# Performance work log

Hardware: AMD Instinct MI355X
Metric: run time of the kernel (lower is better)

The kernel has to match this reference:

```python
import jax, jax.numpy as jnp
import numpy as np
import math

B, T, D_MODEL, N_HEADS = 2, 2048, 2048, 16
D_HEAD = D_MODEL // N_HEADS
ROPE_THETA = 10000.0


def setup_inputs() -> dict:
    key = jax.random.key(0)
    ks = jax.random.split(key, 4)
    x = jax.random.normal(ks[0], (B, T, D_MODEL), dtype=jnp.float32)
    # causal mask: True = masked (matches torch masked_fill semantics)
    mask = jnp.triu(jnp.ones((T, T), dtype=bool), k=1)[None, None]  # [1,1,T,T]
    # rotary freqs: complex freqs_cis = exp(i * t * theta^(-2j/d)) -> cos/sin parts
    inv_freq = 1.0 / (ROPE_THETA ** (jnp.arange(0, D_HEAD, 2, dtype=jnp.float32) / D_HEAD))
    angles = jnp.arange(T, dtype=jnp.float32)[:, None] * inv_freq[None, :]  # [T, D_HEAD//2]
    freqs_cos = jnp.cos(angles)
    freqs_sin = jnp.sin(angles)
    s = 1.0 / math.sqrt(D_MODEL)
    Wqkv = jax.random.normal(ks[1], (D_MODEL, 3 * D_MODEL), dtype=jnp.float32) * s
    bqkv = jnp.zeros((3 * D_MODEL,), dtype=jnp.float32)
    Wproj = jax.random.normal(ks[2], (D_MODEL, D_MODEL), dtype=jnp.float32) * s
    bproj = jnp.zeros((D_MODEL,), dtype=jnp.float32)
    return {"x": x, "mask": mask, "freqs_cos": freqs_cos, "freqs_sin": freqs_sin,
            "Wqkv": Wqkv, "bqkv": bqkv, "Wproj": Wproj, "bproj": bproj}


def _rope(t, cos, sin):
    # t: [B,H,T,D]; cos/sin: [1,1,T,D//2]. Complex multiply on (even, odd) pairs.
    t2 = t.reshape(*t.shape[:-1], -1, 2)
    t_re, t_im = t2[..., 0], t2[..., 1]
    out_re = t_re * cos - t_im * sin
    out_im = t_re * sin + t_im * cos
    return jnp.stack([out_re, out_im], axis=-1).reshape(t.shape)


def reference(x, mask, freqs_cos, freqs_sin, Wqkv, bqkv, Wproj, bproj):
    Bb, Tt, C = x.shape
    qkv = x @ Wqkv + bqkv                                   # [B,T,3C]
    q, k, v = jnp.split(qkv, 3, axis=-1)
    def heads(t):
        return t.reshape(Bb, Tt, N_HEADS, D_HEAD).transpose(0, 2, 1, 3)  # [B,H,T,D]
    q, k, v = heads(q), heads(k), heads(v)
    cos = freqs_cos[None, None]                              # [1,1,T,D//2]
    sin = freqs_sin[None, None]
    q = _rope(q, cos, sin)
    k = _rope(k, cos, sin)
    att = jnp.einsum('bhqd,bhkd->bhqk', q, k) / math.sqrt(D_HEAD)
    att = jnp.where(mask, -jnp.inf, att)
    att = jax.nn.softmax(att, axis=-1)
    # attn_dropout is identity in eval mode
    out = jnp.einsum('bhqk,bhkd->bhqd', att, v)              # [B,H,T,D]
    out = out.transpose(0, 2, 1, 3).reshape(Bb, Tt, C)
    return (out @ Wproj + bproj, k, v)
```

## Files before the change

kernel.cpp:

```cpp
#include <hip/hip_runtime.h>
#include <hip/hip_bf16.h>

#define T_SEQ 2048
#define DM    2048
#define NH    16
#define DH    128
#define NBH   32
#define MROWS 4096

typedef __bf16 bf16x8 __attribute__((ext_vector_type(8)));
typedef __bf16 bf16x4 __attribute__((ext_vector_type(4)));
typedef float  f32x4  __attribute__((ext_vector_type(4)));

#define MFMA16 __builtin_amdgcn_mfma_f32_16x16x32_bf16

__device__ __forceinline__ void async_copy16(const void* g, void* l) {
  __builtin_amdgcn_global_load_lds((const __attribute__((address_space(1))) void*)g,
                                   (__attribute__((address_space(3))) void*)l, 16, 0, 0);
}


__global__ void cast_bf16_k(const float* __restrict__ x, __bf16* __restrict__ xb) {
  int i = (blockIdx.x * 256 + threadIdx.x) * 4;
  float4 v = *reinterpret_cast<const float4*>(x + i);
  bf16x4 o;
  o[0] = (__bf16)v.x; o[1] = (__bf16)v.y; o[2] = (__bf16)v.z; o[3] = (__bf16)v.w;
  *reinterpret_cast<bf16x4*>(xb + i) = o;
}

__global__ void transpose_cast_w(const float* __restrict__ W, __bf16* __restrict__ WT,
                                 int K, int N) {
  __shared__ float tile[32][33];
  int n0 = blockIdx.x * 32, k0 = blockIdx.y * 32;
  int tx = threadIdx.x, ty = threadIdx.y;
  #pragma unroll
  for (int i = 0; i < 4; i++)
    tile[ty + i * 8][tx] = W[(size_t)(k0 + ty + i * 8) * N + n0 + tx];
  __syncthreads();
  #pragma unroll
  for (int i = 0; i < 4; i++)
    WT[(size_t)(n0 + ty + i * 8) * K + k0 + tx] = (__bf16)tile[tx][ty + i * 8];
}

__global__ void transpose_v(const __bf16* __restrict__ Vb, __bf16* __restrict__ Vtb) {
  __shared__ __bf16 tile[32][34];
  int t0 = blockIdx.x * 32, d0 = blockIdx.y * 32, bh = blockIdx.z;
  const __bf16* src = Vb + (size_t)bh * T_SEQ * DH;
  __bf16* dst = Vtb + (size_t)bh * DH * T_SEQ;
  int tx = threadIdx.x, ty = threadIdx.y;
  #pragma unroll
  for (int i = 0; i < 4; i++)
    tile[ty + i * 8][tx] = src[(size_t)(t0 + ty + i * 8) * DH + d0 + tx];
  __syncthreads();
  #pragma unroll
  for (int i = 0; i < 4; i++)
    dst[(size_t)(d0 + ty + i * 8) * T_SEQ + t0 + tx] = tile[tx][ty + i * 8];
}


__device__ __forceinline__ bf16x8 rds(const __bf16* base, int row, int chunk) {
  return *reinterpret_cast<const bf16x8*>(
      reinterpret_cast<const char*>(base) + row * 128 + ((chunk ^ (row & 7)) << 4));
}

__device__ __forceinline__ void stage64(const __bf16* g, int K, int kt, char* lds,
                                        int wave, int lane) {
  #pragma unroll
  for (int j = 0; j < 4; j++) {
    int r = wave * 32 + j * 8 + (lane >> 3);
    int c = lane & 7;
    const char* src = (const char*)g + (size_t)r * (K * 2) + kt * 128 + ((c ^ (r & 7)) << 4);
    async_copy16(src, lds + wave * 4096 + j * 1024);
  }
}

template <int EPI>
__global__ __launch_bounds__(256, 2) void gemm_bt(
    const __bf16* __restrict__ A, const __bf16* __restrict__ Bt, int K,
    const float* __restrict__ bias,
    const float* __restrict__ fcos, const float* __restrict__ fsin,
    __bf16* __restrict__ Qb, __bf16* __restrict__ Kb, __bf16* __restrict__ Vb,
    float* __restrict__ kout, float* __restrict__ vout,
    float* __restrict__ outp) {
  __shared__ __align__(16) char smem[65536];
  const int tid = threadIdx.x, lane = tid & 63, wave = tid >> 6;
  const int hi = lane >> 4, lo = lane & 15;
  const int wm = (wave >> 1) * 64, wn = (wave & 1) * 64;
  const __bf16* Ab = A + (size_t)blockIdx.y * 128 * K;
  const __bf16* Bb = Bt + (size_t)blockIdx.x * 128 * K;
  f32x4 acc[4][4] = {};
  const int NK = K >> 6;

  stage64(Ab, K, 0, smem, wave, lane);
  stage64(Bb, K, 0, smem + 32768, wave, lane);
  __syncthreads();

  for (int t = 0; t < NK; ++t) {
    const int sel = (t & 1) ? 16384 : 0;
    const __bf16* Ac = (const __bf16*)(smem + sel);
    const __bf16* Bc = (const __bf16*)(smem + 32768 + sel);
    if (t + 1 < NK) {
      stage64(Ab, K, t + 1, smem + (sel ^ 16384), wave, lane);
      stage64(Bb, K, t + 1, smem + 32768 + (sel ^ 16384), wave, lane);
    }
    bf16x8 a0[4], b0[4], a1[4], b1[4];
    #pragma unroll
    for (int m = 0; m < 4; ++m) a0[m] = rds(Ac, wm + m * 16 + lo, hi);
    #pragma unroll
    for (int n = 0; n < 4; ++n) b0[n] = rds(Bc, wn + n * 16 + lo, hi);
    __builtin_amdgcn_s_setprio(1);
    #pragma unroll
    for (int m = 0; m < 4; ++m)
      #pragma unroll
      for (int n = 0; n < 4; ++n)
        acc[m][n] = MFMA16(a0[m], b0[n], acc[m][n], 0, 0, 0);
    __builtin_amdgcn_s_setprio(0);
    #pragma unroll
    for (int m = 0; m < 4; ++m) a1[m] = rds(Ac, wm + m * 16 + lo, 4 + hi);
    #pragma unroll
    for (int n = 0; n < 4; ++n) b1[n] = rds(Bc, wn + n * 16 + lo, 4 + hi);
    __builtin_amdgcn_s_setprio(1);
    #pragma unroll
    for (int m = 0; m < 4; ++m)
      #pragma unroll
      for (int n = 0; n < 4; ++n)
        acc[m][n] = MFMA16(a1[m], b1[n], acc[m][n], 0, 0, 0);
    __builtin_amdgcn_s_setprio(0);
    __syncthreads();
  }

  float* sc = (float*)smem;
  const int rl_r = tid >> 3;
  const int cb   = (tid & 7) * 16;
  #pragma unroll
  for (int cc = 0; cc < 4; ++cc) {
    __syncthreads();
    if ((wave >> 1) == (cc >> 1)) {
      #pragma unroll
      for (int mm = 0; mm < 2; ++mm) {
        int m = (cc & 1) * 2 + mm;
        #pragma unroll
        for (int j = 0; j < 4; ++j) {
          int col = wn + j * 16 + lo;
          int rl = mm * 16 + hi * 4;
          #pragma unroll
          for (int r = 0; r < 4; ++r)
            sc[(rl + r) * 132 + col] = acc[m][j][r];
        }
      }
    }
    __syncthreads();
    float v[16];
    #pragma unroll
    for (int q = 0; q < 4; ++q)
      *reinterpret_cast<float4*>(&v[q * 4]) =
          *reinterpret_cast<const float4*>(&sc[rl_r * 132 + cb + q * 4]);
    const int row = blockIdx.y * 128 + cc * 32 + rl_r;
    const int n0  = blockIdx.x * 128 + cb;
    #pragma unroll
    for (int q = 0; q < 4; ++q) {
      float4 bv = *reinterpret_cast<const float4*>(&bias[n0 + q * 4]);
      v[q * 4 + 0] += bv.x; v[q * 4 + 1] += bv.y;
      v[q * 4 + 2] += bv.z; v[q * 4 + 3] += bv.w;
    }
    if (EPI == 1) {
      const int which = n0 >> 11;
      const int wn2 = n0 & 2047, h = wn2 >> 7, d0 = wn2 & 127;
      const int b = row >> 11, tt = row & 2047;
      if (which < 2) {
        const float* cp = fcos + tt * 64 + (d0 >> 1);
        const float* sp = fsin + tt * 64 + (d0 >> 1);
        float4 c0 = *reinterpret_cast<const float4*>(cp);
        float4 c1 = *reinterpret_cast<const float4*>(cp + 4);
        float4 s0 = *reinterpret_cast<const float4*>(sp);
        float4 s1 = *reinterpret_cast<const float4*>(sp + 4);
        float cs[8] = {c0.x, c0.y, c0.z, c0.w, c1.x, c1.y, c1.z, c1.w};
        float sn[8] = {s0.x, s0.y, s0.z, s0.w, s1.x, s1.y, s1.z, s1.w};
        #pragma unroll
        for (int p = 0; p < 8; ++p) {
          float re = v[2 * p], im = v[2 * p + 1];
          v[2 * p]     = re * cs[p] - im * sn[p];
          v[2 * p + 1] = re * sn[p] + im * cs[p];
        }
      }
      size_t base = (((size_t)(b * NH + h)) * T_SEQ + tt) * DH + d0;
      bf16x8 o0, o1;
      #pragma unroll
      for (int p = 0; p < 8; ++p) { o0[p] = (__bf16)v[p]; o1[p] = (__bf16)v[8 + p]; }
      if (which == 0) {
        *reinterpret_cast<bf16x8*>(Qb + base) = o0;
        *reinterpret_cast<bf16x8*>(Qb + base + 8) = o1;
      } else if (which == 1) {
        *reinterpret_cast<bf16x8*>(Kb + base) = o0;
        *reinterpret_cast<bf16x8*>(Kb + base + 8) = o1;
        #pragma unroll
        for (int q = 0; q < 4; ++q)
          *reinterpret_cast<float4*>(kout + base + q * 4) =
              *reinterpret_cast<const float4*>(&v[q * 4]);
      } else {
        *reinterpret_cast<bf16x8*>(Vb + base) = o0;
        *reinterpret_cast<bf16x8*>(Vb + base + 8) = o1;
        #pragma unroll
        for (int q = 0; q < 4; ++q)
          *reinterpret_cast<float4*>(vout + base + q * 4) =
              *reinterpret_cast<const float4*>(&v[q * 4]);
      }
    } else {
      float* op = outp + (size_t)row * DM + n0;
      #pragma unroll
      for (int q = 0; q < 4; ++q)
        *reinterpret_cast<float4*>(op + q * 4) =
            *reinterpret_cast<const float4*>(&v[q * 4]);
    }
  }
}


__device__ __forceinline__ bf16x8 lds_frag(const __bf16* base, int row, int chunk) {
  return *reinterpret_cast<const bf16x8*>(
      reinterpret_cast<const char*>(base) + row * 256 + ((chunk ^ (row & 7)) << 4));
}

__device__ __forceinline__ void stage64x256(const __bf16* g, __bf16* lds, int tid) {
  const int wave = tid >> 6, lane = tid & 63;
  #pragma unroll
  for (int j = 0; j < 4; j++) {
    int off = j * 4096 + wave * 1024;
    int r = (off >> 8) + (lane >> 4);
    int c = lane & 15;
    const char* gs = (const char*)g + (size_t)r * 256 + ((c ^ (r & 7)) << 4);
    async_copy16(gs, (char*)lds + off);
  }
}

__device__ __forceinline__ void stage128x128(const __bf16* g, size_t rstrideB, int colB,
                                             __bf16* lds, int tid) {
  const int wave = tid >> 6, lane = tid & 63;
  #pragma unroll
  for (int j = 0; j < 4; j++) {
    int off = j * 4096 + wave * 1024;
    int r = (off >> 7) + (lane >> 3);
    int c = lane & 7;
    const char* gs = (const char*)g + (size_t)r * rstrideB + colB + ((c ^ (r & 7)) << 4);
    async_copy16(gs, (char*)lds + off);
  }
}

__global__ __launch_bounds__(256, 2) void attn_fwd(
    const __bf16* __restrict__ Qb, const __bf16* __restrict__ Kb,
    const __bf16* __restrict__ Vtb, __bf16* __restrict__ att_out) {
  __shared__ __bf16 Ks[64 * 128];
  __shared__ __bf16 Vts[128 * 64];
  __shared__ __bf16 Ps[4 * 16 * 64];
  const int tid = threadIdx.x, lane = tid & 63, wave = tid >> 6;
  const int hi = lane >> 4, lo = lane & 15;
  const int linear = (int)blockIdx.x;
  const int xcd = linear & 7, rest = linear >> 3;
  const int bh = xcd + 8 * (rest >> 4);
  const int pair = rest & 15;
  const int b = bh >> 4, h = bh & 15;
  const __bf16* Qg = Qb + (size_t)bh * T_SEQ * DH;
  const __bf16* Kg = Kb + (size_t)bh * T_SEQ * DH;
  const __bf16* Vg = Vtb + (size_t)bh * DH * T_SEQ;
  const float scale = 0.08838834764831845f;
  const float L2E = 1.4426950408889634f;
  __bf16* Pw = Ps + wave * 1024;

  for (int pass = 0; pass < 2; ++pass) {
    const int qj = pass ? (31 - pair) : pair;
    const int q0 = qj * 64;
    const int qg = q0 + wave * 16 + lo;
    bf16x8 qf[4];
    const __bf16* qp = Qg + (size_t)qg * DH + hi * 8;
    #pragma unroll
    for (int ks = 0; ks < 4; ++ks) qf[ks] = *reinterpret_cast<const bf16x8*>(qp + ks * 32);
    f32x4 oacc[8] = {};
    float m = -3e38f, l = 0.f;
    const int NT = qj + 1;

    for (int kt = 0; kt < NT; ++kt) {
      __syncthreads();
      stage64x256(Kg + (size_t)kt * 64 * DH, Ks, tid);
      stage128x128(Vg, (size_t)T_SEQ * 2, kt * 128, Vts, tid);
      __syncthreads();

      f32x4 sacc[4] = {};
      __builtin_amdgcn_s_setprio(1);
      #pragma unroll
      for (int ks = 0; ks < 4; ++ks)
        #pragma unroll
        for (int sf = 0; sf < 4; ++sf) {
          bf16x8 ak = lds_frag(Ks, sf * 16 + lo, ks * 4 + hi);
          sacc[sf] = MFMA16(ak, qf[ks], sacc[sf], 0, 0, 0);
        }
      __builtin_amdgcn_s_setprio(0);
      const bool diag = (kt == NT - 1);
      float mx = -3e38f;
      #pragma unroll
      for (int sf = 0; sf < 4; ++sf)
        #pragma unroll
        for (int r = 0; r < 4; ++r) {
          float v = sacc[sf][r] * scale;
          if (diag && (kt * 64 + sf * 16 + hi * 4 + r) > qg) v = -3e38f;
          sacc[sf][r] = v;
          mx = fmaxf(mx, v);
        }
      mx = fmaxf(mx, __shfl_xor(mx, 16, 64));
      mx = fmaxf(mx, __shfl_xor(mx, 32, 64));
      const bool nr = __all(mx - m <= 8.0f);
      if (!nr) {
        float mnew = fmaxf(m, mx);
        float alpha = __builtin_exp2f((m - mnew) * L2E);
        m = mnew;
        l *= alpha;
        #pragma unroll
        for (int df = 0; df < 8; ++df) {
          oacc[df][0] *= alpha; oacc[df][1] *= alpha;
          oacc[df][2] *= alpha; oacc[df][3] *= alpha;
        }
      }
      float rs = 0.f;
      #pragma unroll
      for (int sf = 0; sf < 4; ++sf)
        #pragma unroll
        for (int r = 0; r < 4; ++r) {
          float p = __builtin_exp2f((sacc[sf][r] - m) * L2E);
          sacc[sf][r] = p;
          rs += p;
        }
      rs += __shfl_xor(rs, 16, 64);
      rs += __shfl_xor(rs, 32, 64);
      l += rs;
      #pragma unroll
      for (int sf = 0; sf < 4; ++sf) {
        bf16x4 pk;
        pk[0] = (__bf16)sacc[sf][0]; pk[1] = (__bf16)sacc[sf][1];
        pk[2] = (__bf16)sacc[sf][2]; pk[3] = (__bf16)sacc[sf][3];
        int byte = sf * 32 + hi * 8;
        int chunk = byte >> 4, rem = byte & 15;
        char* p = (char*)Pw + lo * 128 + (((chunk ^ (lo & 7)) << 4) | rem);
        *reinterpret_cast<bf16x4*>(p) = pk;
      }
      __builtin_amdgcn_s_setprio(1);
      #pragma unroll
      for (int ks = 0; ks < 2; ++ks) {
        bf16x8 bp = rds(Pw, lo, ks * 4 + hi);
        #pragma unroll
        for (int df = 0; df < 8; ++df) {
          bf16x8 av = rds(Vts, df * 16 + lo, ks * 4 + hi);
          oacc[df] = MFMA16(av, bp, oacc[df], 0, 0, 0);
        }
      }
      __builtin_amdgcn_s_setprio(0);
    }

    float inv = 1.0f / l;
    int qrow = b * T_SEQ + q0 + wave * 16 + lo;
    #pragma unroll
    for (int df = 0; df < 8; ++df) {
      bf16x4 pk;
      pk[0] = (__bf16)(oacc[df][0] * inv);
      pk[1] = (__bf16)(oacc[df][1] * inv);
      pk[2] = (__bf16)(oacc[df][2] * inv);
      pk[3] = (__bf16)(oacc[df][3] * inv);
      int d = df * 16 + hi * 4;
      *reinterpret_cast<bf16x4*>(att_out + (size_t)qrow * DM + h * DH + d) = pk;
    }
  }
}


extern "C" void kernel_launch(void* const* d_in, const int* in_sizes, int n_in,
                              void* d_out, int out_size, void* d_ws, size_t ws_size,
                              hipStream_t stream) {
  const float* x     = (const float*)d_in[0];
  const float* fcos  = (const float*)d_in[2];
  const float* fsin  = (const float*)d_in[3];
  const float* Wqkv  = (const float*)d_in[4];
  const float* bqkv  = (const float*)d_in[5];
  const float* Wproj = (const float*)d_in[6];
  const float* bproj = (const float*)d_in[7];
  float* out  = (float*)d_out;
  float* kout = out + (size_t)8388608;
  float* vout = out + (size_t)16777216;

  char* ws = (char*)d_ws;
  __bf16* xb     = (__bf16*)(ws);
  __bf16* WqkvT  = (__bf16*)(ws + 16777216);
  __bf16* WprojT = (__bf16*)(ws + 41943040);
  __bf16* Qb     = (__bf16*)(ws + 50331648);
  __bf16* Kb     = (__bf16*)(ws + 67108864);
  __bf16* Vb     = (__bf16*)(ws + 83886080);
  __bf16* Vtb    = (__bf16*)(ws + 100663296);
  __bf16* att    = xb;

  cast_bf16_k<<<8192, 256, 0, stream>>>(x, xb);
  transpose_cast_w<<<dim3(192, 64), dim3(32, 8), 0, stream>>>(Wqkv, WqkvT, DM, 3 * DM);
  transpose_cast_w<<<dim3(64, 64), dim3(32, 8), 0, stream>>>(Wproj, WprojT, DM, DM);
  gemm_bt<1><<<dim3(48, 32), 256, 0, stream>>>(xb, WqkvT, DM, bqkv, fcos, fsin,
                                               Qb, Kb, Vb, kout, vout, nullptr);
  transpose_v<<<dim3(64, 4, NBH), dim3(32, 8), 0, stream>>>(Vb, Vtb);
  attn_fwd<<<512, 256, 0, stream>>>(Qb, Kb, Vtb, att);
  gemm_bt<0><<<dim3(16, 32), 256, 0, stream>>>(att, WprojT, DM, bproj, nullptr, nullptr,
                                               nullptr, nullptr, nullptr, nullptr, nullptr, out);
}
```

Measured before the change: 281.6 us.

## Prefetch next K/V tile into registers to overlap global loads with compute

Replaces the direct global-to-LDS async copies of each K and V tile with register-staged loads. The next tile is fetched from global memory into registers while the current tile is being computed, then written to LDS at the top of the next iteration. This hides global-memory latency behind the QK and PV MFMA work. In exchange it uses 8 more vector registers per thread for staging, which under the (256,2) launch bounds could cause spills, and it adds explicit LDS store instructions.

```diff
diff --git a/kernel.cpp b/kernel.cpp
--- a/kernel.cpp
+++ b/kernel.cpp
@@ -221,29 +221,39 @@
       reinterpret_cast<const char*>(base) + row * 256 + ((chunk ^ (row & 7)) << 4));
 }
 
-__device__ __forceinline__ void stage64x256(const __bf16* g, __bf16* lds, int tid) {
-  const int wave = tid >> 6, lane = tid & 63;
+__device__ __forceinline__ void ldK(const __bf16* Kg, int kt, int wave, int lane,
+                                    bf16x8 k[4]) {
+  const char* g = (const char*)(Kg + (size_t)kt * 64 * DH);
   #pragma unroll
   for (int j = 0; j < 4; j++) {
     int off = j * 4096 + wave * 1024;
     int r = (off >> 8) + (lane >> 4);
     int c = lane & 15;
-    const char* gs = (const char*)g + (size_t)r * 256 + ((c ^ (r & 7)) << 4);
-    async_copy16(gs, (char*)lds + off);
-  }
-}
-
-__device__ __forceinline__ void stage128x128(const __bf16* g, size_t rstrideB, int colB,
-                                             __bf16* lds, int tid) {
-  const int wave = tid >> 6, lane = tid & 63;
+    k[j] = *reinterpret_cast<const bf16x8*>(g + (size_t)r * 256 + ((c ^ (r & 7)) << 4));
+  }
+}
+
+__device__ __forceinline__ void ldV(const __bf16* Vg, int kt, int wave, int lane,
+                                    bf16x8 v[4]) {
+  const char* g = (const char*)Vg;
+  const int colB = kt * 128;
   #pragma unroll
   for (int j = 0; j < 4; j++) {
     int off = j * 4096 + wave * 1024;
     int r = (off >> 7) + (lane >> 3);
     int c = lane & 7;
-    const char* gs = (const char*)g + (size_t)r * rstrideB + colB + ((c ^ (r & 7)) << 4);
-    async_copy16(gs, (char*)lds + off);
-  }
+    v[j] = *reinterpret_cast<const bf16x8*>(g + (size_t)r * (T_SEQ * 2) + colB + ((c ^ (r & 7)) << 4));
+  }
+}
+
+__device__ __forceinline__ void commitKV(__bf16* Ks, __bf16* Vts, int wave, int lane,
+                                         const bf16x8 k[4], const bf16x8 v[4]) {
+  #pragma unroll
+  for (int j = 0; j < 4; j++)
+    *reinterpret_cast<bf16x8*>((char*)Ks + j * 4096 + wave * 1024 + lane * 16) = k[j];
+  #pragma unroll
+  for (int j = 0; j < 4; j++)
+    *reinterpret_cast<bf16x8*>((char*)Vts + j * 4096 + wave * 1024 + lane * 16) = v[j];
 }
 
 __global__ __launch_bounds__(256, 2) void attn_fwd(
@@ -278,11 +288,18 @@
     float m = -3e38f, l = 0.f;
     const int NT = qj + 1;
 
+    bf16x8 kst[4], vst[4];
+    ldK(Kg, 0, wave, lane, kst);
+    ldV(Vg, 0, wave, lane, vst);
+
     for (int kt = 0; kt < NT; ++kt) {
       __syncthreads();
-      stage64x256(Kg + (size_t)kt * 64 * DH, Ks, tid);
-      stage128x128(Vg, (size_t)T_SEQ * 2, kt * 128, Vts, tid);
+      commitKV(Ks, Vts, wave, lane, kst, vst);
       __syncthreads();
+      if (kt + 1 < NT) {
+        ldK(Kg, kt + 1, wave, lane, kst);
+        ldV(Vg, kt + 1, wave, lane, vst);
+      }
 
       f32x4 sacc[4] = {};
       __builtin_amdgcn_s_setprio(1);
```

After: 276.9 us. About the same (-1.7%).

## Give each attention wave two query fragments and split query tiles across blocks

Applied to the files above, without the earlier changes.

The attention kernel now launches 1024 blocks of 2 waves instead of 512 blocks of 4 waves. Each wave handles 32 query rows as two 16-row fragments, so every K and V fragment read from LDS feeds two MFMAs. Each block processes one query tile instead of a balanced pair of tiles, with slot interleaving used to spread causal work. This aims to cut LDS read traffic per MFMA, at the cost of more registers per wave, fewer waves to share each staging step, and possibly worse load balance since blocks now carry uneven causal work.

```diff
diff --git a/kernel.cpp b/kernel.cpp
--- a/kernel.cpp
+++ b/kernel.cpp
@@ -221,11 +221,10 @@
       reinterpret_cast<const char*>(base) + row * 256 + ((chunk ^ (row & 7)) << 4));
 }
 
-__device__ __forceinline__ void stage64x256(const __bf16* g, __bf16* lds, int tid) {
-  const int wave = tid >> 6, lane = tid & 63;
-  #pragma unroll
-  for (int j = 0; j < 4; j++) {
-    int off = j * 4096 + wave * 1024;
+__device__ __forceinline__ void stageK(const __bf16* g, __bf16* lds, int wave, int lane) {
+  #pragma unroll
+  for (int j = 0; j < 8; j++) {
+    int off = j * 2048 + wave * 1024;
     int r = (off >> 8) + (lane >> 4);
     int c = lane & 15;
     const char* gs = (const char*)g + (size_t)r * 256 + ((c ^ (r & 7)) << 4);
@@ -233,136 +232,153 @@
   }
 }
 
-__device__ __forceinline__ void stage128x128(const __bf16* g, size_t rstrideB, int colB,
-                                             __bf16* lds, int tid) {
-  const int wave = tid >> 6, lane = tid & 63;
-  #pragma unroll
-  for (int j = 0; j < 4; j++) {
-    int off = j * 4096 + wave * 1024;
+__device__ __forceinline__ void stageV(const __bf16* g, int kt, __bf16* lds,
+                                       int wave, int lane) {
+  #pragma unroll
+  for (int j = 0; j < 8; j++) {
+    int off = j * 2048 + wave * 1024;
     int r = (off >> 7) + (lane >> 3);
     int c = lane & 7;
-    const char* gs = (const char*)g + (size_t)r * rstrideB + colB + ((c ^ (r & 7)) << 4);
+    const char* gs = (const char*)g + (size_t)r * (T_SEQ * 2) + kt * 128 + ((c ^ (r & 7)) << 4);
     async_copy16(gs, (char*)lds + off);
   }
 }
 
-__global__ __launch_bounds__(256, 2) void attn_fwd(
+__global__ __launch_bounds__(128, 2) void attn_fwd(
     const __bf16* __restrict__ Qb, const __bf16* __restrict__ Kb,
     const __bf16* __restrict__ Vtb, __bf16* __restrict__ att_out) {
   __shared__ __bf16 Ks[64 * 128];
   __shared__ __bf16 Vts[128 * 64];
-  __shared__ __bf16 Ps[4 * 16 * 64];
+  __shared__ __bf16 Ps[2 * 32 * 64];
   const int tid = threadIdx.x, lane = tid & 63, wave = tid >> 6;
   const int hi = lane >> 4, lo = lane & 15;
   const int linear = (int)blockIdx.x;
   const int xcd = linear & 7, rest = linear >> 3;
-  const int bh = xcd + 8 * (rest >> 4);
-  const int pair = rest & 15;
+  const int slot = rest & 31;
+  const int bh = xcd + 8 * (rest >> 5);
+  const int qj = (slot & 1) ? (31 - (slot >> 1)) : (slot >> 1);
   const int b = bh >> 4, h = bh & 15;
   const __bf16* Qg = Qb + (size_t)bh * T_SEQ * DH;
   const __bf16* Kg = Kb + (size_t)bh * T_SEQ * DH;
   const __bf16* Vg = Vtb + (size_t)bh * DH * T_SEQ;
   const float scale = 0.08838834764831845f;
   const float L2E = 1.4426950408889634f;
-  __bf16* Pw = Ps + wave * 1024;
-
-  for (int pass = 0; pass < 2; ++pass) {
-    const int qj = pass ? (31 - pair) : pair;
-    const int q0 = qj * 64;
-    const int qg = q0 + wave * 16 + lo;
-    bf16x8 qf[4];
-    const __bf16* qp = Qg + (size_t)qg * DH + hi * 8;
-    #pragma unroll
-    for (int ks = 0; ks < 4; ++ks) qf[ks] = *reinterpret_cast<const bf16x8*>(qp + ks * 32);
-    f32x4 oacc[8] = {};
-    float m = -3e38f, l = 0.f;
-    const int NT = qj + 1;
-
-    for (int kt = 0; kt < NT; ++kt) {
-      __syncthreads();
-      stage64x256(Kg + (size_t)kt * 64 * DH, Ks, tid);
-      stage128x128(Vg, (size_t)T_SEQ * 2, kt * 128, Vts, tid);
-      __syncthreads();
-
-      f32x4 sacc[4] = {};
-      __builtin_amdgcn_s_setprio(1);
-      #pragma unroll
-      for (int ks = 0; ks < 4; ++ks)
-        #pragma unroll
-        for (int sf = 0; sf < 4; ++sf) {
-          bf16x8 ak = lds_frag(Ks, sf * 16 + lo, ks * 4 + hi);
-          sacc[sf] = MFMA16(ak, qf[ks], sacc[sf], 0, 0, 0);
-        }
-      __builtin_amdgcn_s_setprio(0);
-      const bool diag = (kt == NT - 1);
+  __bf16* Pw = Ps + wave * 2048;
+
+  const int q0 = qj * 64;
+  const int qg0 = q0 + wave * 32 + lo;
+  const int qg1 = qg0 + 16;
+  bf16x8 qf0[4], qf1[4];
+  {
+    const __bf16* qp0 = Qg + (size_t)qg0 * DH + hi * 8;
+    const __bf16* qp1 = Qg + (size_t)qg1 * DH + hi * 8;
+    #pragma unroll
+    for (int ks = 0; ks < 4; ++ks) {
+      qf0[ks] = *reinterpret_cast<const bf16x8*>(qp0 + ks * 32);
+      qf1[ks] = *reinterpret_cast<const bf16x8*>(qp1 + ks * 32);
+    }
+  }
+  f32x4 oacc[8][2] = {};
+  float m0 = -3e38f, m1 = -3e38f, l0 = 0.f, l1 = 0.f;
+  const int NT = qj + 1;
+
+  for (int kt = 0; kt < NT; ++kt) {
+    __syncthreads();
+    stageK(Kg + (size_t)kt * 64 * DH, Ks, wave, lane);
+    stageV(Vg, kt, Vts, wave, lane);
+    __syncthreads();
+
+    f32x4 sacc[4][2] = {};
+    __builtin_amdgcn_s_setprio(1);
+    #pragma unroll
+    for (int ks = 0; ks < 4; ++ks)
+      #pragma unroll
+      for (int sf = 0; sf < 4; ++sf) {
+        bf16x8 ak = lds_frag(Ks, sf * 16 + lo, ks * 4 + hi);
+        sacc[sf][0] = MFMA16(ak, qf0[ks], sacc[sf][0], 0, 0, 0);
+        sacc[sf][1] = MFMA16(ak, qf1[ks], sacc[sf][1], 0, 0, 0);
+      }
+    __builtin_amdgcn_s_setprio(0);
+    const bool diag = (kt == NT - 1);
+    #pragma unroll
+    for (int qf = 0; qf < 2; ++qf) {
+      const int qgl = qf ? qg1 : qg0;
+      float mold = qf ? m1 : m0;
       float mx = -3e38f;
       #pragma unroll
       for (int sf = 0; sf < 4; ++sf)
         #pragma unroll
         for (int r = 0; r < 4; ++r) {
-          float v = sacc[sf][r] * scale;
-          if (diag && (kt * 64 + sf * 16 + hi * 4 + r) > qg) v = -3e38f;
-          sacc[sf][r] = v;
+          float v = sacc[sf][qf][r] * scale;
+          if (diag && (kt * 64 + sf * 16 + hi * 4 + r) > qgl) v = -3e38f;
+          sacc[sf][qf][r] = v;
           mx = fmaxf(mx, v);
         }
       mx = fmaxf(mx, __shfl_xor(mx, 16, 64));
       mx = fmaxf(mx, __shfl_xor(mx, 32, 64));
-      const bool nr = __all(mx - m <= 8.0f);
+      const bool nr = __all(mx - mold <= 8.0f);
       if (!nr) {
-        float mnew = fmaxf(m, mx);
-        float alpha = __builtin_exp2f((m - mnew) * L2E);
-        m = mnew;
-        l *= alpha;
+        float mnew = fmaxf(mold, mx);
+        float alpha = __builtin_exp2f((mold - mnew) * L2E);
+        mold = mnew;
+        if (qf) l1 *= alpha; else l0 *= alpha;
         #pragma unroll
         for (int df = 0; df < 8; ++df) {
-          oacc[df][0] *= alpha; oacc[df][1] *= alpha;
-          oacc[df][2] *= alpha; oacc[df][3] *= alpha;
+          oacc[df][qf][0] *= alpha; oacc[df][qf][1] *= alpha;
+          oacc[df][qf][2] *= alpha; oacc[df][qf][3] *= alpha;
         }
       }
+      if (qf) m1 = mold; else m0 = mold;
       float rs = 0.f;
       #pragma unroll
       for (int sf = 0; sf < 4; ++sf)
         #pragma unroll
         for (int r = 0; r < 4; ++r) {
-          float p = __builtin_exp2f((sacc[sf][r] - m) * L2E);
-          sacc[sf][r] = p;
+          float p = __builtin_exp2f((sacc[sf][qf][r] - mold) * L2E);
+          sacc[sf][qf][r] = p;
           rs += p;
         }
       rs += __shfl_xor(rs, 16, 64);
       rs += __shfl_xor(rs, 32, 64);
-      l += rs;
+      if (qf) l1 += rs; else l0 += rs;
+      const int q_loc = qf * 16 + lo;
       #pragma unroll
       for (int sf = 0; sf < 4; ++sf) {
         bf16x4 pk;
-        pk[0] = (__bf16)sacc[sf][0]; pk[1] = (__bf16)sacc[sf][1];
-        pk[2] = (__bf16)sacc[sf][2]; pk[3] = (__bf16)sacc[sf][3];
+        pk[0] = (__bf16)sacc[sf][qf][0]; pk[1] = (__bf16)sacc[sf][qf][1];
+        pk[2] = (__bf16)sacc[sf][qf][2]; pk[3] = (__bf16)sacc[sf][qf][3];
         int byte = sf * 32 + hi * 8;
         int chunk = byte >> 4, rem = byte & 15;
-        char* p = (char*)Pw + lo * 128 + (((chunk ^ (lo & 7)) << 4) | rem);
+        char* p = (char*)Pw + q_loc * 128 + (((chunk ^ (q_loc & 7)) << 4) | rem);
         *reinterpret_cast<bf16x4*>(p) = pk;
       }
-      __builtin_amdgcn_s_setprio(1);
-      #pragma unroll
-      for (int ks = 0; ks < 2; ++ks) {
-        bf16x8 bp = rds(Pw, lo, ks * 4 + hi);
-        #pragma unroll
-        for (int df = 0; df < 8; ++df) {
-          bf16x8 av = rds(Vts, df * 16 + lo, ks * 4 + hi);
-          oacc[df] = MFMA16(av, bp, oacc[df], 0, 0, 0);
-        }
-      }
-      __builtin_amdgcn_s_setprio(0);
-    }
-
-    float inv = 1.0f / l;
-    int qrow = b * T_SEQ + q0 + wave * 16 + lo;
+    }
+    __builtin_amdgcn_s_setprio(1);
+    #pragma unroll
+    for (int ks = 0; ks < 2; ++ks) {
+      bf16x8 bp0 = rds(Pw, lo, ks * 4 + hi);
+      bf16x8 bp1 = rds(Pw, 16 + lo, ks * 4 + hi);
+      #pragma unroll
+      for (int df = 0; df < 8; ++df) {
+        bf16x8 av = rds(Vts, df * 16 + lo, ks * 4 + hi);
+        oacc[df][0] = MFMA16(av, bp0, oacc[df][0], 0, 0, 0);
+        oacc[df][1] = MFMA16(av, bp1, oacc[df][1], 0, 0, 0);
+      }
+    }
+    __builtin_amdgcn_s_setprio(0);
+  }
+
+  #pragma unroll
+  for (int qf = 0; qf < 2; ++qf) {
+    float inv = 1.0f / (qf ? l1 : l0);
+    int qrow = b * T_SEQ + q0 + wave * 32 + qf * 16 + lo;
     #pragma unroll
     for (int df = 0; df < 8; ++df) {
       bf16x4 pk;
-      pk[0] = (__bf16)(oacc[df][0] * inv);
-      pk[1] = (__bf16)(oacc[df][1] * inv);
-      pk[2] = (__bf16)(oacc[df][2] * inv);
-      pk[3] = (__bf16)(oacc[df][3] * inv);
+      pk[0] = (__bf16)(oacc[df][qf][0] * inv);
+      pk[1] = (__bf16)(oacc[df][qf][1] * inv);
+      pk[2] = (__bf16)(oacc[df][qf][2] * inv);
+      pk[3] = (__bf16)(oacc[df][qf][3] * inv);
       int d = df * 16 + hi * 4;
       *reinterpret_cast<bf16x4*>(att_out + (size_t)qrow * DM + h * DH + d) = pk;
     }
@@ -400,7 +416,7 @@
   gemm_bt<1><<<dim3(48, 32), 256, 0, stream>>>(xb, WqkvT, DM, bqkv, fcos, fsin,
                                                Qb, Kb, Vb, kout, vout, nullptr);
   transpose_v<<<dim3(64, 4, NBH), dim3(32, 8), 0, stream>>>(Vb, Vtb);
-  attn_fwd<<<512, 256, 0, stream>>>(Qb, Kb, Vtb, att);
+  attn_fwd<<<1024, 128, 0, stream>>>(Qb, Kb, Vtb, att);
   gemm_bt<0><<<dim3(16, 32), 256, 0, stream>>>(att, WprojT, DM, bproj, nullptr, nullptr,
                                                nullptr, nullptr, nullptr, nullptr, nullptr, out);
 }
```

New measurement: 320.1 us. 13.7% more time.
